# Optimization experiments

Measured on AMD Instinct MI355X. Metric: run time of the kernel, lower is better.

## Reference

```python
import jax, jax.numpy as jnp
import numpy as np

LAYERS = 8
K = 2  # kernel size


def _causal_conv(x, w, b, dilation):
    # x: [B, C, T]; w: [Cout, Cin, K] (torch OIW layout); b: [Cout]
    pad = (K - 1) * dilation
    y = jax.lax.conv_general_dilated(
        x, w,
        window_strides=(1,),
        padding=[(pad, 0)],
        rhs_dilation=(dilation,),
        dimension_numbers=("NCH", "OIH", "NCH"),
    )
    return y + b[None, :, None]


def setup_inputs() -> dict:
    key = jax.random.key(0)
    ks = jax.random.split(key, 5)
    B, C, T = 16, 256, 4096
    scale = 1.0 / np.sqrt(C * K)
    return {
        "ys": jax.random.normal(ks[0], (B, C, T), dtype=jnp.float32),
        "filters_w": jax.random.normal(ks[1], (LAYERS, C, C, K), dtype=jnp.float32) * scale,
        "filters_b": jax.random.normal(ks[2], (LAYERS, C), dtype=jnp.float32) * scale,
        "gates_w": jax.random.normal(ks[3], (LAYERS, C, C, K), dtype=jnp.float32) * scale,
        "gates_b": jax.random.normal(ks[4], (LAYERS, C), dtype=jnp.float32) * scale,
    }


def reference(ys, filters_w, filters_b, gates_w, gates_b):
    Zs = ys
    Zout = jnp.zeros_like(ys)
    for l in range(LAYERS):
        d = 2 ** l
        F_ = jnp.tanh(_causal_conv(Zs, filters_w[l], filters_b[l], d))
        G_ = jax.nn.sigmoid(_causal_conv(Zs, gates_w[l], gates_b[l], d))
        Zs = F_ * G_
        Zout = Zout + Zs
    return Zout
```

## Files before the change

### kernel.cpp

```cpp
#include <hip/hip_runtime.h>


typedef __attribute__((ext_vector_type(8))) short s16x8;
typedef __attribute__((ext_vector_type(4))) short s16x4;
typedef __attribute__((ext_vector_type(4))) float f32x4;

#define NB 16
#define NC 256
#define NT 4096
#define TPAD 4224
#define PADT 128
#define NLAYERS 8
#define KTOT 512
#define MSTK 512

__device__ __forceinline__ short f2bf(float x) {
  union { float f; unsigned u; } v; v.f = x;
  unsigned u = v.u;
  unsigned r = (u + 0x7fffu + ((u >> 16) & 1u)) >> 16;
  return (short)r;
}
__device__ __forceinline__ float bf2f(short s) {
  union { float f; unsigned u; } v; v.u = ((unsigned)(unsigned short)s) << 16;
  return v.f;
}

__device__ __forceinline__ void async16(short* lp, const short* gp) {
  __builtin_amdgcn_global_load_lds(
      (const __attribute__((address_space(1))) unsigned int*)gp,
      (__attribute__((address_space(3))) unsigned int*)lp,
      16, 0, 0);
}


__global__ void zero_pads(short* __restrict__ base, int nbuf, size_t strideSh) {
  int idx = blockIdx.x * 256 + threadIdx.x;
  if (idx >= nbuf * NB * PADT * NC) return;
  int j = idx >> 19;
  int rem = idx & 524287;
  int b = rem >> 15;
  int r2 = rem & 32767;
  base[(size_t)j * strideSh + (size_t)b * TPAD * NC + r2] = 0;
}

__global__ void transpose_cast(const float* __restrict__ ys, short* __restrict__ X0) {
  __shared__ float tile[64][65];
  const int b = blockIdx.z, c0 = blockIdx.y * 64, t0 = blockIdx.x * 64;
  const int tid = threadIdx.x;
#pragma unroll
  for (int i = 0; i < 16; ++i) {
    int c = (tid >> 6) + i * 4;
    int t = tid & 63;
    tile[c][t] = ys[((size_t)(b * NC + c0 + c)) * NT + t0 + t];
  }
  __syncthreads();
#pragma unroll
  for (int i = 0; i < 2; ++i) {
    int q = tid + i * 256;
    int t = q >> 3, cc = (q & 7) * 8;
    s16x8 v;
#pragma unroll
    for (int j = 0; j < 8; ++j) v[j] = f2bf(tile[cc + j][t]);
    *(s16x8*)&X0[((size_t)(b * TPAD + PADT + t0 + t)) * NC + c0 + cc] = v;
  }
}

__global__ void convert_w(const float* __restrict__ fw, const float* __restrict__ gw,
                          short* __restrict__ Ws) {
  int idx = blockIdx.x * 256 + threadIdx.x;
  if (idx >= NLAYERS * MSTK * KTOT) return;
  int k = idx & (KTOT - 1);
  int r = (idx >> 9) & (MSTK - 1);
  int l = idx >> 18;
  int kw = k >> 8, ci = k & 255;
  int j = r >> 5, s = (r >> 4) & 1, c16 = r & 15;
  int ch = j * 16 + c16;
  int src = ((l * NC + ch) * NC + ci) * 2 + kw;
  Ws[idx] = f2bf(s ? gw[src] : fw[src]);
}

__global__ __launch_bounds__(512, 2)
void wavenet_layer(const short* __restrict__ Xin, short* __restrict__ Xout,
                   const short* __restrict__ Wl,
                   const float* __restrict__ bia_f, const float* __restrict__ bia_g,
                   float* __restrict__ Z, int d, int zmode, int writeX) {
  __shared__ short lds[32768];

  const int tid = threadIdx.x;
  const int wave = tid >> 6, lane = tid & 63;
  const int quad = lane >> 4, l16 = lane & 15;
  const int wm = wave >> 2, wn = wave & 3;

  int flat = blockIdx.x + 2 * (blockIdx.y + 16 * blockIdx.z);
  int swz = (flat & 7) * 64 + (flat >> 3);
  const int mt = swz & 1;
  const int ty = (swz >> 1) & 15;
  const int b  = swz >> 5;
  const int m0s = mt * 256;
  const int t0  = ty * 256;

  const short* Wm = Wl + (size_t)m0s * KTOT;
  const short* Xb = Xin + ((size_t)b * TPAD + PADT + t0) * NC;

  f32x4 acc[8][4] = {};
  const int xo = (quad ^ ((l16 >> 1) & 3)) * 8;

  auto STAGE = [&](int buf, int kk) {
    short* Ad = lds + buf * 8192;
    short* Bd = lds + 16384 + buf * 8192;
    const int kw = kk >> 3;
    const int ci0 = (kk & 7) * 32;
    const int k0 = kw * 256 + ci0;
    const int tsh = (kw == 0) ? -d : 0;
#pragma unroll
    for (int i = 0; i < 2; ++i) {
      int q = (i * 8 + wave) * 64 + lane;
      int r = q >> 2;
      int kc = ((q & 3) ^ ((r >> 1) & 3)) * 8;
      async16(Ad + q * 8, Wm + r * KTOT + k0 + kc);
      async16(Bd + q * 8, Xb + (r + tsh) * NC + ci0 + kc);
    }
  };

  STAGE(0, 0);
  STAGE(1, 1);
  asm volatile("s_waitcnt vmcnt(4)" ::: "memory");
  __builtin_amdgcn_sched_barrier(0);
  __builtin_amdgcn_s_barrier();

  int cur = 0;
#pragma unroll 2
  for (int kk = 0; kk < 16; ++kk) {
    const short* Ar = lds + cur * 8192;
    const short* Br = lds + 16384 + cur * 8192;
    s16x8 bfr[4];
#pragma unroll
    for (int ni = 0; ni < 4; ++ni)
      bfr[ni] = *(const s16x8*)&Br[(wn * 64 + ni * 16 + l16) * 32 + xo];
    __builtin_amdgcn_s_setprio(1);
#pragma unroll
    for (int mi = 0; mi < 8; ++mi) {
      s16x8 af = *(const s16x8*)&Ar[(wm * 128 + mi * 16 + l16) * 32 + xo];
#pragma unroll
      for (int ni = 0; ni < 4; ++ni)
        acc[mi][ni] = __builtin_amdgcn_mfma_f32_16x16x32_bf16(af, bfr[ni], acc[mi][ni], 0, 0, 0);
    }
    __builtin_amdgcn_s_setprio(0);
    if (kk == 15) break;
    asm volatile("s_waitcnt lgkmcnt(0)" ::: "memory");
    __builtin_amdgcn_sched_barrier(0);
    __builtin_amdgcn_s_barrier();
    __builtin_amdgcn_sched_barrier(0);
    if (kk < 14) {
      STAGE(cur, kk + 2);
      asm volatile("s_waitcnt vmcnt(4)" ::: "memory");
    } else {
      asm volatile("s_waitcnt vmcnt(0)" ::: "memory");
    }
    __builtin_amdgcn_sched_barrier(0);
    __builtin_amdgcn_s_barrier();
    __builtin_amdgcn_sched_barrier(0);
    cur ^= 1;
  }
  __syncthreads();

  const int zacc = (zmode == 1 || zmode == 2);
  const int stageZT = (writeX || zacc);
  short* ZT = lds;

#pragma unroll
  for (int p = 0; p < 4; ++p) {
    const int cloc = (wm * 4 + p) * 16 + quad * 4;
    const int ch = mt * 128 + cloc;
    float4 bf4 = *(const float4*)&bia_f[ch];
    float4 bg4 = *(const float4*)&bia_g[ch];
    const float* bfp = (const float*)&bf4;
    const float* bgp = (const float*)&bg4;
#pragma unroll
    for (int ni = 0; ni < 4; ++ni) {
      const int tl = wn * 64 + ni * 16 + l16;
      const int t = t0 + tl;
      short pk[4];
#pragma unroll
      for (int r = 0; r < 4; ++r) {
        float f = acc[2 * p][ni][r] + bfp[r];
        float g = acc[2 * p + 1][ni][r] + bgp[r];
        float ef = __expf(2.f * f);
        float th = 1.f - 2.f / (ef + 1.f);
        float sg = 1.f / (1.f + __expf(-g));
        float z = th * sg;
        if (zmode >= 3) {
          size_t zo = ((size_t)(b * NC + ch + r)) * NT + t;
          if (zmode == 3) Z[zo] = z; else Z[zo] += z;
        }
        pk[r] = f2bf(z);
      }
      if (stageZT) {
        short* dst = &ZT[tl * 128 + ((cloc + tl * 8) & 127)];
        *(s16x4*)dst = (s16x4){pk[0], pk[1], pk[2], pk[3]};
      }
    }
  }
  if (stageZT) {
    __syncthreads();
#pragma unroll
    for (int i = 0; i < 8; ++i) {
      int q = tid + i * 512;
      int t = q >> 4, cc = (q & 15) * 8;
      s16x8 v = *(const s16x8*)&ZT[t * 128 + ((cc + t * 8) & 127)];
      if (writeX)
        *(s16x8*)&Xout[((size_t)(b * TPAD + PADT + t0 + t)) * NC + mt * 128 + cc] = v;
      if (zacc) {
        s16x8 xv = *(const s16x8*)&Xin[((size_t)(b * TPAD + PADT + t0 + t)) * NC + mt * 128 + cc];
        size_t zo = ((size_t)b * NT + t0 + t) * NC + mt * 128 + cc;
        float zv[8];
#pragma unroll
        for (int j = 0; j < 8; ++j) zv[j] = bf2f(v[j]) + bf2f(xv[j]);
        if (zmode == 2) {
          float4 a0 = *(const float4*)&Z[zo];
          float4 a1 = *(const float4*)&Z[zo + 4];
          zv[0] += a0.x; zv[1] += a0.y; zv[2] += a0.z; zv[3] += a0.w;
          zv[4] += a1.x; zv[5] += a1.y; zv[6] += a1.z; zv[7] += a1.w;
        }
        *(float4*)&Z[zo]     = make_float4(zv[0], zv[1], zv[2], zv[3]);
        *(float4*)&Z[zo + 4] = make_float4(zv[4], zv[5], zv[6], zv[7]);
      }
    }
  }
}

__global__ void transpose_out(const float* __restrict__ src, float* __restrict__ dst) {
  __shared__ float tile[64][65];
  const int b = blockIdx.z, c0 = blockIdx.y * 64, t0 = blockIdx.x * 64;
  const int tid = threadIdx.x;
#pragma unroll
  for (int i = 0; i < 4; ++i) {
    int q = tid + i * 256;
    int t = q >> 4, c = (q & 15) * 4;
    float4 v = *(const float4*)&src[((size_t)b * NT + t0 + t) * NC + c0 + c];
    tile[t][c] = v.x; tile[t][c + 1] = v.y; tile[t][c + 2] = v.z; tile[t][c + 3] = v.w;
  }
  __syncthreads();
#pragma unroll
  for (int i = 0; i < 4; ++i) {
    int q = tid + i * 256;
    int c = q >> 4, t = (q & 15) * 4;
    float4 v = make_float4(tile[t][c], tile[t + 1][c], tile[t + 2][c], tile[t + 3][c]);
    *(float4*)&dst[((size_t)b * NC + c0 + c) * NT + t0 + t] = v;
  }
}

__global__ void copy4(const float4* __restrict__ s, float4* __restrict__ d, int n) {
  int i = blockIdx.x * 256 + threadIdx.x;
  int stride = gridDim.x * 256;
  for (; i < n; i += stride) d[i] = s[i];
}

extern "C" void kernel_launch(void* const* d_in, const int* in_sizes, int n_in,
                              void* d_out, int out_size, void* d_ws, size_t ws_size,
                              hipStream_t stream) {
  const float* ys = (const float*)d_in[0];
  const float* fw = (const float*)d_in[1];
  const float* fb = (const float*)d_in[2];
  const float* gw = (const float*)d_in[3];
  const float* gb = (const float*)d_in[4];
  float* Zout = (float*)d_out;

  char* ws = (char*)d_ws;
  const size_t xbytes = (size_t)NB * TPAD * NC * 2;
  const size_t strideSh = xbytes / 2;
  const size_t wbytes = (size_t)NLAYERS * MSTK * KTOT * 2;
  const size_t zbytes = (size_t)NB * NC * NT * 4;

  int tier;
  if (ws_size >= 2 * xbytes + wbytes + zbytes)      tier = 1;
  else if (ws_size >= 2 * xbytes + wbytes)          tier = 2;
  else                                              tier = 3;

  short* Xbase = (short*)ws;
  short* Ws = (short*)(ws + 2 * xbytes);
  float* Zacc = (tier == 1) ? (float*)(ws + 2 * xbytes + wbytes) : Zout;

  {
    int total = 2 * NB * PADT * NC;
    hipLaunchKernelGGL(zero_pads, dim3((total + 255) / 256), dim3(256), 0, stream,
                       Xbase, 2, strideSh);
  }
  hipLaunchKernelGGL(transpose_cast, dim3(64, 4, 16), dim3(256), 0, stream, ys, Xbase);
  hipLaunchKernelGGL(convert_w, dim3(8192), dim3(256), 0, stream, fw, gw, Ws);

  for (int l = 0; l < NLAYERS; ++l) {
    const short* Xin = (l & 1) ? Xbase + strideSh : Xbase;
    short* Xo       = (l & 1) ? Xbase : Xbase + strideSh;
    int writeX = (l < NLAYERS - 1) ? 1 : 0;
    int zmode;
    float* Zp;
    if (tier <= 2) {
      zmode = (l & 1) ? ((l == 1) ? 1 : 2) : 0;
      Zp = Zacc;
    } else {
      zmode = (l == 0) ? 3 : 4;
      Zp = Zout;
    }
    hipLaunchKernelGGL(wavenet_layer, dim3(2, 16, 16), dim3(512), 0, stream,
                       Xin, Xo,
                       Ws + (size_t)l * MSTK * KTOT,
                       fb + l * NC, gb + l * NC, Zp, 1 << l, zmode, writeX);
  }

  if (tier == 1) {
    hipLaunchKernelGGL(transpose_out, dim3(64, 4, 16), dim3(256), 0, stream,
                       Zacc, Zout);
  } else if (tier == 2) {
    float* tmp = (float*)ws;
    hipLaunchKernelGGL(transpose_out, dim3(64, 4, 16), dim3(256), 0, stream,
                       Zacc, tmp);
    int n4 = (int)(zbytes / 16);
    hipLaunchKernelGGL(copy4, dim3(2048), dim3(256), 0, stream,
                       (const float4*)tmp, (float4*)Zout, n4);
  }
}
```

Baseline: 663.6 us.

## Shrink layer tiles to 128x128 and accumulate output every three layers

The per-layer GEMM tile drops from 256x256 with 512 threads to 128x128 with 256 threads, which quadruples the grid and halves LDS per block. The point is better CU occupancy and less load imbalance. The fp32 output accumulation now uses a third bf16 activation buffer, so Z is read and written only at layers 2, 5 and 7 (three layers summed at a time) instead of every other layer. Smaller tiles reload more weight and activation data per FLOP, and the fallback tier now always goes through the transpose path.

```diff
diff --git a/kernel.cpp b/kernel.cpp
--- a/kernel.cpp
+++ b/kernel.cpp
@@ -79,42 +79,43 @@
   Ws[idx] = f2bf(s ? gw[src] : fw[src]);
 }
 
-__global__ __launch_bounds__(512, 2)
+__global__ __launch_bounds__(256, 2)
 void wavenet_layer(const short* __restrict__ Xin, short* __restrict__ Xout,
                    const short* __restrict__ Wl,
                    const float* __restrict__ bia_f, const float* __restrict__ bia_g,
-                   float* __restrict__ Z, int d, int zmode, int writeX) {
-  __shared__ short lds[32768];
+                   float* __restrict__ Z, const short* __restrict__ Xprev,
+                   int d, int zmode, int writeX) {
+  __shared__ short lds[16384];
 
   const int tid = threadIdx.x;
   const int wave = tid >> 6, lane = tid & 63;
   const int quad = lane >> 4, l16 = lane & 15;
-  const int wm = wave >> 2, wn = wave & 3;
-
-  int flat = blockIdx.x + 2 * (blockIdx.y + 16 * blockIdx.z);
-  int swz = (flat & 7) * 64 + (flat >> 3);
-  const int mt = swz & 1;
-  const int ty = (swz >> 1) & 15;
-  const int b  = swz >> 5;
-  const int m0s = mt * 256;
-  const int t0  = ty * 256;
+  const int wm = wave >> 1, wn = wave & 1;
+
+  int flat = blockIdx.x + 4 * (blockIdx.y + 32 * blockIdx.z);
+  int swz = (flat & 7) * 256 + (flat >> 3);
+  const int mt = swz & 3;
+  const int ty = (swz >> 2) & 31;
+  const int b  = swz >> 7;
+  const int m0s = mt * 128;
+  const int t0  = ty * 128;
 
   const short* Wm = Wl + (size_t)m0s * KTOT;
   const short* Xb = Xin + ((size_t)b * TPAD + PADT + t0) * NC;
 
-  f32x4 acc[8][4] = {};
+  f32x4 acc[4][4] = {};
   const int xo = (quad ^ ((l16 >> 1) & 3)) * 8;
 
   auto STAGE = [&](int buf, int kk) {
-    short* Ad = lds + buf * 8192;
-    short* Bd = lds + 16384 + buf * 8192;
+    short* Ad = lds + buf * 4096;
+    short* Bd = lds + 8192 + buf * 4096;
     const int kw = kk >> 3;
     const int ci0 = (kk & 7) * 32;
     const int k0 = kw * 256 + ci0;
     const int tsh = (kw == 0) ? -d : 0;
 #pragma unroll
     for (int i = 0; i < 2; ++i) {
-      int q = (i * 8 + wave) * 64 + lane;
+      int q = i * 256 + tid;
       int r = q >> 2;
       int kc = ((q & 3) ^ ((r >> 1) & 3)) * 8;
       async16(Ad + q * 8, Wm + r * KTOT + k0 + kc);
@@ -131,16 +132,16 @@
   int cur = 0;
 #pragma unroll 2
   for (int kk = 0; kk < 16; ++kk) {
-    const short* Ar = lds + cur * 8192;
-    const short* Br = lds + 16384 + cur * 8192;
+    const short* Ar = lds + cur * 4096;
+    const short* Br = lds + 8192 + cur * 4096;
     s16x8 bfr[4];
 #pragma unroll
     for (int ni = 0; ni < 4; ++ni)
       bfr[ni] = *(const s16x8*)&Br[(wn * 64 + ni * 16 + l16) * 32 + xo];
     __builtin_amdgcn_s_setprio(1);
 #pragma unroll
-    for (int mi = 0; mi < 8; ++mi) {
-      s16x8 af = *(const s16x8*)&Ar[(wm * 128 + mi * 16 + l16) * 32 + xo];
+    for (int mi = 0; mi < 4; ++mi) {
+      s16x8 af = *(const s16x8*)&Ar[(wm * 64 + mi * 16 + l16) * 32 + xo];
 #pragma unroll
       for (int ni = 0; ni < 4; ++ni)
         acc[mi][ni] = __builtin_amdgcn_mfma_f32_16x16x32_bf16(af, bfr[ni], acc[mi][ni], 0, 0, 0);
@@ -164,14 +165,12 @@
   }
   __syncthreads();
 
-  const int zacc = (zmode == 1 || zmode == 2);
-  const int stageZT = (writeX || zacc);
   short* ZT = lds;
 
 #pragma unroll
-  for (int p = 0; p < 4; ++p) {
-    const int cloc = (wm * 4 + p) * 16 + quad * 4;
-    const int ch = mt * 128 + cloc;
+  for (int p = 0; p < 2; ++p) {
+    const int cloc = (wm * 2 + p) * 16 + quad * 4;
+    const int ch = mt * 64 + cloc;
     float4 bf4 = *(const float4*)&bia_f[ch];
     float4 bg4 = *(const float4*)&bia_g[ch];
     const float* bfp = (const float*)&bf4;
@@ -179,7 +178,6 @@
 #pragma unroll
     for (int ni = 0; ni < 4; ++ni) {
       const int tl = wn * 64 + ni * 16 + l16;
-      const int t = t0 + tl;
       short pk[4];
 #pragma unroll
       for (int r = 0; r < 4; ++r) {
@@ -188,43 +186,39 @@
         float ef = __expf(2.f * f);
         float th = 1.f - 2.f / (ef + 1.f);
         float sg = 1.f / (1.f + __expf(-g));
-        float z = th * sg;
-        if (zmode >= 3) {
-          size_t zo = ((size_t)(b * NC + ch + r)) * NT + t;
-          if (zmode == 3) Z[zo] = z; else Z[zo] += z;
-        }
-        pk[r] = f2bf(z);
+        pk[r] = f2bf(th * sg);
       }
-      if (stageZT) {
-        short* dst = &ZT[tl * 128 + ((cloc + tl * 8) & 127)];
-        *(s16x4*)dst = (s16x4){pk[0], pk[1], pk[2], pk[3]};
+      short* dst = &ZT[tl * 64 + ((cloc + tl * 8) & 63)];
+      *(s16x4*)dst = (s16x4){pk[0], pk[1], pk[2], pk[3]};
+    }
+  }
+  __syncthreads();
+#pragma unroll
+  for (int i = 0; i < 4; ++i) {
+    int q = tid + i * 256;
+    int t = q >> 3, cc = (q & 7) * 8;
+    s16x8 v = *(const s16x8*)&ZT[t * 64 + ((cc + t * 8) & 63)];
+    const size_t xoff = ((size_t)(b * TPAD + PADT + t0 + t)) * NC + mt * 64 + cc;
+    if (writeX) *(s16x8*)&Xout[xoff] = v;
+    if (zmode) {
+      s16x8 xv = *(const s16x8*)&Xin[xoff];
+      float zv[8];
+#pragma unroll
+      for (int j = 0; j < 8; ++j) zv[j] = bf2f(v[j]) + bf2f(xv[j]);
+      if (Xprev) {
+        s16x8 pv = *(const s16x8*)&Xprev[xoff];
+#pragma unroll
+        for (int j = 0; j < 8; ++j) zv[j] += bf2f(pv[j]);
       }
-    }
-  }
-  if (stageZT) {
-    __syncthreads();
-#pragma unroll
-    for (int i = 0; i < 8; ++i) {
-      int q = tid + i * 512;
-      int t = q >> 4, cc = (q & 15) * 8;
-      s16x8 v = *(const s16x8*)&ZT[t * 128 + ((cc + t * 8) & 127)];
-      if (writeX)
-        *(s16x8*)&Xout[((size_t)(b * TPAD + PADT + t0 + t)) * NC + mt * 128 + cc] = v;
-      if (zacc) {
-        s16x8 xv = *(const s16x8*)&Xin[((size_t)(b * TPAD + PADT + t0 + t)) * NC + mt * 128 + cc];
-        size_t zo = ((size_t)b * NT + t0 + t) * NC + mt * 128 + cc;
-        float zv[8];
-#pragma unroll
-        for (int j = 0; j < 8; ++j) zv[j] = bf2f(v[j]) + bf2f(xv[j]);
-        if (zmode == 2) {
-          float4 a0 = *(const float4*)&Z[zo];
-          float4 a1 = *(const float4*)&Z[zo + 4];
-          zv[0] += a0.x; zv[1] += a0.y; zv[2] += a0.z; zv[3] += a0.w;
-          zv[4] += a1.x; zv[5] += a1.y; zv[6] += a1.z; zv[7] += a1.w;
-        }
-        *(float4*)&Z[zo]     = make_float4(zv[0], zv[1], zv[2], zv[3]);
-        *(float4*)&Z[zo + 4] = make_float4(zv[4], zv[5], zv[6], zv[7]);
+      size_t zo = ((size_t)b * NT + t0 + t) * NC + mt * 64 + cc;
+      if (zmode == 2) {
+        float4 a0 = *(const float4*)&Z[zo];
+        float4 a1 = *(const float4*)&Z[zo + 4];
+        zv[0] += a0.x; zv[1] += a0.y; zv[2] += a0.z; zv[3] += a0.w;
+        zv[4] += a1.x; zv[5] += a1.y; zv[6] += a1.z; zv[7] += a1.w;
       }
+      *(float4*)&Z[zo]     = make_float4(zv[0], zv[1], zv[2], zv[3]);
+      *(float4*)&Z[zo + 4] = make_float4(zv[4], zv[5], zv[6], zv[7]);
     }
   }
 }
@@ -273,45 +267,52 @@
   const size_t zbytes = (size_t)NB * NC * NT * 4;
 
   int tier;
-  if (ws_size >= 2 * xbytes + wbytes + zbytes)      tier = 1;
-  else if (ws_size >= 2 * xbytes + wbytes)          tier = 2;
+  if (ws_size >= 3 * xbytes + wbytes + zbytes)      tier = 1;
+  else if (ws_size >= 3 * xbytes + wbytes)          tier = 2;
   else                                              tier = 3;
 
+  const int nxb = (tier <= 2) ? 3 : 2;
   short* Xbase = (short*)ws;
-  short* Ws = (short*)(ws + 2 * xbytes);
-  float* Zacc = (tier == 1) ? (float*)(ws + 2 * xbytes + wbytes) : Zout;
+  short* Ws = (short*)(ws + nxb * xbytes);
+  float* Zacc = (tier == 1) ? (float*)(ws + 3 * xbytes + wbytes) : Zout;
 
   {
-    int total = 2 * NB * PADT * NC;
+    int total = nxb * NB * PADT * NC;
     hipLaunchKernelGGL(zero_pads, dim3((total + 255) / 256), dim3(256), 0, stream,
-                       Xbase, 2, strideSh);
+                       Xbase, nxb, strideSh);
   }
   hipLaunchKernelGGL(transpose_cast, dim3(64, 4, 16), dim3(256), 0, stream, ys, Xbase);
   hipLaunchKernelGGL(convert_w, dim3(8192), dim3(256), 0, stream, fw, gw, Ws);
 
   for (int l = 0; l < NLAYERS; ++l) {
-    const short* Xin = (l & 1) ? Xbase + strideSh : Xbase;
-    short* Xo       = (l & 1) ? Xbase : Xbase + strideSh;
+    const short* Xin;
+    short* Xo;
+    int zmode;
+    const short* Xprev = nullptr;
+    if (tier <= 2) {
+      Xin = Xbase + (size_t)(l % 3) * strideSh;
+      Xo  = Xbase + (size_t)((l + 1) % 3) * strideSh;
+      if (l == 2)      { zmode = 1; Xprev = Xbase + strideSh; }
+      else if (l == 5) { zmode = 2; Xprev = Xbase + strideSh; }
+      else if (l == 7) { zmode = 2; }
+      else             { zmode = 0; }
+    } else {
+      Xin = (l & 1) ? Xbase + strideSh : Xbase;
+      Xo  = (l & 1) ? Xbase : Xbase + strideSh;
+      zmode = (l & 1) ? ((l == 1) ? 1 : 2) : 0;
+    }
     int writeX = (l < NLAYERS - 1) ? 1 : 0;
-    int zmode;
-    float* Zp;
-    if (tier <= 2) {
-      zmode = (l & 1) ? ((l == 1) ? 1 : 2) : 0;
-      Zp = Zacc;
-    } else {
-      zmode = (l == 0) ? 3 : 4;
-      Zp = Zout;
-    }
-    hipLaunchKernelGGL(wavenet_layer, dim3(2, 16, 16), dim3(512), 0, stream,
+    hipLaunchKernelGGL(wavenet_layer, dim3(4, 32, 16), dim3(256), 0, stream,
                        Xin, Xo,
                        Ws + (size_t)l * MSTK * KTOT,
-                       fb + l * NC, gb + l * NC, Zp, 1 << l, zmode, writeX);
+                       fb + l * NC, gb + l * NC, Zacc, Xprev,
+                       1 << l, zmode, writeX);
   }
 
   if (tier == 1) {
     hipLaunchKernelGGL(transpose_out, dim3(64, 4, 16), dim3(256), 0, stream,
                        Zacc, Zout);
-  } else if (tier == 2) {
+  } else {
     float* tmp = (float*)ws;
     hipLaunchKernelGGL(transpose_out, dim3(64, 4, 16), dim3(256), 0, stream,
                        Zacc, tmp);
```

Result: faster. 545.6 us (-17.8%).
